# Optimization experiments

Measured on AMD Instinct MI355X. Metric: run time of the kernel, lower is better.

The kernel has to match this reference:

```python
import jax, jax.numpy as jnp
import numpy as np

B, T, D = 2, 2048, 1024
NH, DH = 16, 64  # inner = NH*DH = D
SCALE_INIT = 0.02


def setup_inputs() -> dict:
    key = jax.random.key(0)
    kx, kq, kk, kv, ko = jax.random.split(key, 5)
    return {
        "x": jax.random.normal(kx, (B, T, D), dtype=jnp.float32),
        "Wq": jax.random.normal(kq, (D, NH * DH), dtype=jnp.float32) * SCALE_INIT,
        "Wk": jax.random.normal(kk, (D, NH * DH), dtype=jnp.float32) * SCALE_INIT,
        "Wv": jax.random.normal(kv, (D, NH * DH), dtype=jnp.float32) * SCALE_INIT,
        "Wo": jax.random.normal(ko, (NH * DH, D), dtype=jnp.float32) * SCALE_INIT,
    }


def reference(x, Wq, Wk, Wv, Wo):
    # x: (B, T, D)
    b, t, _ = x.shape

    def split_heads(h):
        # (B, T, NH*DH) -> (B, NH, T, DH)
        return h.reshape(b, t, NH, DH).transpose(0, 2, 1, 3)

    q = split_heads(x @ Wq)
    k = split_heads(x @ Wk)
    v = split_heads(x @ Wv)

    scale = jnp.asarray(1.0 / np.sqrt(DH), dtype=x.dtype)
    # The per-chunk loop in the original is mathematically equivalent to
    # full causal attention: each query row attends to keys with k_pos <= q_pos.
    scores = jnp.einsum("bhqd,bhkd->bhqk", q, k) * scale  # (B, NH, T, T)
    causal_mask = jnp.arange(t)[None, :] > jnp.arange(t)[:, None]  # k_pos > q_pos
    scores = jnp.where(causal_mask, -jnp.inf, scores)
    attn = jax.nn.softmax(scores, axis=-1)
    attn = jnp.nan_to_num(attn)  # matches torch.nan_to_num (no fully-masked rows in causal case)
    o = jnp.einsum("bhqk,bhkd->bhqd", attn, v)  # (B, NH, T, DH)
    o = o.transpose(0, 2, 1, 3).reshape(b, t, NH * DH)  # merge heads
    return o @ Wo  # (B, T, D)
```

## Files before the change

### kernel.cpp

```cpp
#include <hip/hip_runtime.h>
#include <hip/hip_bf16.h>
#include <string.h>

#define Bsz 2
#define Tsz 2048
#define Dsz 1024
#define NHsz 16
#define Msz (Bsz*Tsz)

typedef unsigned short bfu;
typedef __attribute__((ext_vector_type(8))) short short8;
typedef __attribute__((ext_vector_type(4))) short short4v;
typedef __attribute__((ext_vector_type(4))) float floatx4;

__device__ __forceinline__ bfu f2bf(float f) {
  unsigned int u = __builtin_bit_cast(unsigned int, f);
  u += 0x7fffu + ((u >> 16) & 1u);
  return (bfu)(u >> 16);
}

__device__ __forceinline__ float fexp2(float x) {
#if __has_builtin(__builtin_amdgcn_exp2f)
  return __builtin_amdgcn_exp2f(x);
#else
  return exp2f(x);
#endif
}

__device__ __forceinline__ short4v pack4bf(float a, float b, float c_, float d) {
  __hip_bfloat162 h01 = __float22bfloat162_rn(make_float2(a, b));
  __hip_bfloat162 h23 = __float22bfloat162_rn(make_float2(c_, d));
  uint2 uu;
  memcpy(&uu.x, &h01, 4);
  memcpy(&uu.y, &h23, 4);
  return __builtin_bit_cast(short4v, uu);
}

__device__ __forceinline__ short8 pack8bf(float4 a, float4 b) {
  __hip_bfloat162 h0 = __float22bfloat162_rn(make_float2(a.x, a.y));
  __hip_bfloat162 h1 = __float22bfloat162_rn(make_float2(a.z, a.w));
  __hip_bfloat162 h2 = __float22bfloat162_rn(make_float2(b.x, b.y));
  __hip_bfloat162 h3 = __float22bfloat162_rn(make_float2(b.z, b.w));
  uint4 u;
  memcpy(&u.x, &h0, 4); memcpy(&u.y, &h1, 4);
  memcpy(&u.z, &h2, 4); memcpy(&u.w, &h3, 4);
  return __builtin_bit_cast(short8, u);
}

__device__ __forceinline__ void async16(const void* g, void* l) {
  void* gnc = (void*)g;
  __builtin_amdgcn_global_load_lds((__attribute__((address_space(1))) void*)gnc,
                                   (__attribute__((address_space(3))) void*)l,
                                   16, 0, 0);
}

__global__ __launch_bounds__(256) void transpose_w(const float* __restrict__ W0, const float* __restrict__ W1,
                                                   const float* __restrict__ W2, const float* __restrict__ W3,
                                                   bfu* __restrict__ wt,
                                                   const float* __restrict__ x, bfu* __restrict__ xb) {
  if (blockIdx.z == 4) {
    const int bf = (int)blockIdx.y * 32 + (int)blockIdx.x;
    const size_t i = ((size_t)bf * 256 + threadIdx.y * 32 + threadIdx.x) * 16;
    float4 a0 = *(const float4*)(x + i),     a1 = *(const float4*)(x + i + 4);
    float4 b0 = *(const float4*)(x + i + 8), b1 = *(const float4*)(x + i + 12);
    *(short8*)(xb + i)     = pack8bf(a0, a1);
    *(short8*)(xb + i + 8) = pack8bf(b0, b1);
    return;
  }
  __shared__ float tile[32][33];
  const float* W = blockIdx.z == 0 ? W0 : blockIdx.z == 1 ? W1 : blockIdx.z == 2 ? W2 : W3;
  const float s = (blockIdx.z == 0) ? 0.18033688011112042f : 1.0f;
  bfu* WT = wt + (size_t)blockIdx.z * Dsz * Dsz;
  int tx = threadIdx.x, ty = threadIdx.y;
  int kb = blockIdx.y * 32, nb = blockIdx.x * 32;
#pragma unroll
  for (int i = 0; i < 4; ++i)
    tile[ty + i*8][tx] = W[(size_t)(kb + ty + i*8) * Dsz + nb + tx];
  __syncthreads();
#pragma unroll
  for (int i = 0; i < 4; ++i)
    WT[(size_t)(nb + ty + i*8) * Dsz + kb + tx] = f2bf(tile[tx][ty + i*8] * s);
}

template <bool F32OUT, int NT>
__global__ __launch_bounds__(256) void gemm128(const bfu* __restrict__ Ain, const bfu* __restrict__ Bt0,
                                               void* __restrict__ C0, int K, int N,
                                               size_t strideB, size_t strideC) {
  constexpr int NJ = NT / 32;
  constexpr int LPS = 2 + NT / 64;
  const int tid = threadIdx.x, wave = tid >> 6, lane = tid & 63;
  const int g = lane >> 4, c = lane & 15;
  const int m0 = blockIdx.y * 128, n0 = blockIdx.x * NT;
  const bfu* Bt = Bt0 + strideB * blockIdx.z;
  __shared__ bfu smem[3][4096 + NT * 32];
  floatx4 acc[4][NJ] = {};
  const int srow = lane >> 2;
  const int scol = (((lane & 3) ^ ((lane >> 3) & 3)) << 3);
  const bfu* gB = Bt + (size_t)(n0 + srow) * K + scol;
  const bfu* gA = Ain + (size_t)(m0 + srow) * K + scol;
  const int wm = (wave >> 1) * 64, wn = (wave & 1) * (NT / 2);
  const int roct = (g ^ ((c >> 1) & 3)) << 3;

#define STAGE_G(buf, k0)                                                        \
  {                                                                             \
    _Pragma("unroll")                                                           \
    for (int cc = 0; cc < 2; ++cc) {                                            \
      const int chunk = wave * 2 + cc;                                          \
      async16(gA + (size_t)chunk * 16 * K + (k0), &smem[buf][chunk * 512]);     \
    }                                                                           \
    _Pragma("unroll")                                                           \
    for (int cc = 0; cc < NT / 64; ++cc) {                                      \
      const int chunk = wave * (NT / 64) + cc;                                  \
      async16(gB + (size_t)chunk * 16 * K + (k0), &smem[buf][4096 + chunk * 512]); \
    }                                                                           \
  }

  const int NK = K / 32;
  STAGE_G(0, 0);
  STAGE_G(1, 32);
  int buf = 0;
  for (int t = 0; t < NK; ++t) {
    if (t + 2 < NK) {
      const int nb = (buf + 2) >= 3 ? buf - 1 : buf + 2;
      STAGE_G(nb, (t + 2) * 32);
      asm volatile("s_waitcnt vmcnt(%0)" :: "i"(2 * LPS) : "memory");
    } else if (t + 1 < NK) {
      asm volatile("s_waitcnt vmcnt(%0)" :: "i"(LPS) : "memory");
    } else {
      asm volatile("s_waitcnt vmcnt(0)" ::: "memory");
    }
    __builtin_amdgcn_s_barrier();
    asm volatile("" ::: "memory");

    const bfu* AsC = &smem[buf][0];
    const bfu* BsC = &smem[buf][4096];
    short8 afr[4], bfr[NJ];
#pragma unroll
    for (int i = 0; i < 4; ++i) afr[i] = *(const short8*)&AsC[(wm + i*16 + c) * 32 + roct];
#pragma unroll
    for (int j = 0; j < NJ; ++j) bfr[j] = *(const short8*)&BsC[(wn + j*16 + c) * 32 + roct];
#pragma unroll
    for (int i = 0; i < 4; ++i)
#pragma unroll
      for (int j = 0; j < NJ; ++j)
        acc[i][j] = __builtin_amdgcn_mfma_f32_16x16x32_bf16(afr[i], bfr[j], acc[i][j], 0, 0, 0);

    asm volatile("" ::: "memory");
    __builtin_amdgcn_s_barrier();
    asm volatile("" ::: "memory");
    buf = (buf + 1 >= 3) ? 0 : buf + 1;
  }
#undef STAGE_G

  const bool vtrans = (!F32OUT) && (NT == 128) && (blockIdx.z == 2);
  if (vtrans) {
    bfu* sm = &smem[0][0];
    bfu* vtp = (bfu*)C0 + (size_t)2 * strideC;
#pragma unroll
    for (int p = 0; p < 2; ++p) {
      __syncthreads();
      if ((wave & 1) == p) {
#pragma unroll
        for (int i = 0; i < 4; ++i)
#pragma unroll
          for (int j = 0; j < NJ; ++j) {
            const int nl = j*16 + c;
            const int mg = ((wm + i*16) >> 3) + (g >> 1);
            const int phys = nl * 128 + ((mg ^ (nl & 15)) << 3) + ((g & 1) << 2);
            *(short4v*)&sm[phys] = pack4bf(acc[i][j][0], acc[i][j][1],
                                           acc[i][j][2], acc[i][j][3]);
          }
      }
      __syncthreads();
      const int h_ = (n0 + p * 64) >> 6;
      bfu* dst = vtp + ((size_t)((m0 >> 11) * 16 + h_) * 64) * Tsz + (m0 & 2047);
#pragma unroll
      for (int s = 0; s < 4; ++s) {
        const int nl = s * 16 + (tid >> 4);
        const int me = (tid & 15) << 3;
        const int phys = nl * 128 + (((me >> 3) ^ (nl & 15)) << 3);
        *(short8*)&dst[(size_t)nl * Tsz + me] = *(const short8*)&sm[phys];
      }
    }
    return;
  }

#pragma unroll
  for (int i = 0; i < 4; ++i) {
#pragma unroll
    for (int j = 0; j < NJ; ++j) {
      const int m = m0 + wm + i*16 + g*4;
      const int n = n0 + wn + j*16 + c;
#pragma unroll
      for (int r = 0; r < 4; ++r) {
        float v = acc[i][j][r];
        if (F32OUT) ((float*)C0)[(size_t)(m + r) * N + n] = v;
        else        ((bfu*)C0)[strideC * blockIdx.z + (size_t)(m + r) * N + n] = f2bf(v);
      }
    }
  }
}

__global__ __launch_bounds__(256, 4) void attn_kernel(const bfu* __restrict__ qkv,
                                                      float* __restrict__ op0,
                                                      float* __restrict__ op1,
                                                      float2* __restrict__ ml) {
  const int tid = threadIdx.x, wave = tid >> 6, lane = tid & 63;
  const int g = (lane >> 4) & 3, c = lane & 15, c7 = c & 7;

  const int flat = (int)blockIdx.y * 32 + (int)blockIdx.x;
  const int xcd = flat & 7, r_ = flat >> 3;
  const int ksplit = r_ & 1;
  const int s = (r_ >> 1) & 3, j0 = r_ >> 3;
  const int bh = xcd * 4 + s;
  const int b = bh >> 4, h = bh & 15;

  const size_t hbq = (size_t)b * Tsz * Dsz + h * 64;
  const bfu* Qp = qkv + hbq;
  const bfu* Kp = qkv + (size_t)Msz * Dsz + hbq;
  const bfu* Vt = qkv + (size_t)2 * Msz * Dsz + (size_t)bh * 64 * Tsz;
  float* op = ksplit ? op1 : op0;

  __shared__ bfu Ks[2][64 * 64];
  __shared__ bfu Vs[2][64 * 64];

  const int srow8 = lane >> 3;
  const int soff = ((lane & 7) ^ srow8) << 3;
  const floatx4 z4 = {0.0f, 0.0f, 0.0f, 0.0f};

  for (int hf = 0; hf < 2; ++hf) {
    const int j = hf ? (31 - j0) : j0;
    const int qw = j * 64 + wave * 16;

    short8 bq[2];
#pragma unroll
    for (int kk = 0; kk < 2; ++kk)
      bq[kk] = *(const short8*)(Qp + (size_t)(qw + c) * Dsz + kk * 32 + g * 8);

    floatx4 acc[4] = {};
    float mi = -3.0e38f, li = 0.0f;

    if (ksplit <= j) {
      const bfu* kpp[2]; const bfu* vpp[2];
#pragma unroll
      for (int cc = 0; cc < 2; ++cc) {
        const int ch = wave * 2 + cc;
        kpp[cc] = Kp + (size_t)(ksplit * 64 + ch * 8 + srow8) * Dsz + soff;
        vpp[cc] = Vt + (size_t)(ch * 8 + srow8) * Tsz + ksplit * 64 + soff;
      }

#pragma unroll
      for (int cc = 0; cc < 2; ++cc) {
        const int ch = wave * 2 + cc;
        async16(kpp[cc], &Ks[0][ch * 512]);
        async16(vpp[cc], &Vs[0][ch * 512]);
        kpp[cc] += (size_t)128 * Dsz;
        vpp[cc] += 128;
      }

      int cur = 0;
      for (int kt = ksplit; kt <= j; kt += 2) {
        if (kt + 2 <= j) {
#pragma unroll
          for (int cc = 0; cc < 2; ++cc) {
            const int ch = wave * 2 + cc;
            async16(kpp[cc], &Ks[cur ^ 1][ch * 512]);
            async16(vpp[cc], &Vs[cur ^ 1][ch * 512]);
            kpp[cc] += (size_t)128 * Dsz;
            vpp[cc] += 128;
          }
          asm volatile("s_waitcnt vmcnt(4)" ::: "memory");
        } else {
          asm volatile("s_waitcnt vmcnt(0)" ::: "memory");
        }
        __builtin_amdgcn_s_barrier();
        asm volatile("" ::: "memory");

        const bfu* KsC = &Ks[cur][0];
        const bfu* VsC = &Vs[cur][0];

        floatx4 st[4];
        __builtin_amdgcn_s_setprio(1);
#pragma unroll
        for (int mk = 0; mk < 4; ++mk) {
          const short8 kf = *(const short8*)&KsC[(mk * 16 + c) * 64 + ((g ^ c7) << 3)];
          st[mk] = __builtin_amdgcn_mfma_f32_16x16x32_bf16(kf, bq[0], z4, 0, 0, 0);
        }
#pragma unroll
        for (int mk = 0; mk < 4; ++mk) {
          const short8 kf = *(const short8*)&KsC[(mk * 16 + c) * 64 + (((4 + g) ^ c7) << 3)];
          st[mk] = __builtin_amdgcn_mfma_f32_16x16x32_bf16(kf, bq[1], st[mk], 0, 0, 0);
        }
        __builtin_amdgcn_s_setprio(0);

        if (kt == j) {
#pragma unroll
          for (int mk = 0; mk < 4; ++mk) {
            const int keyb = kt * 64 + mk * 16 + g * 4;
#pragma unroll
            for (int r = 0; r < 4; ++r)
              if (keyb + r > qw + c) st[mk][r] = -1.0e38f;
          }
        }

        float mloc = -3.0e38f;
#pragma unroll
        for (int mk = 0; mk < 4; ++mk)
          mloc = fmaxf(mloc, fmaxf(fmaxf(st[mk][0], st[mk][1]),
                                   fmaxf(st[mk][2], st[mk][3])));
        const bool resc = !__all(mloc <= mi + 8.0f);
        if (resc) {
          float mr = fmaxf(mloc, __shfl_xor(mloc, 16));
          mr = fmaxf(mr, __shfl_xor(mr, 32));
          const float mnew = fmaxf(mi, mr);
          const float alpha = fexp2(mi - mnew);
          li *= alpha;
          mi = mnew;
          float al[4];
#pragma unroll
          for (int rr = 0; rr < 4; ++rr) al[rr] = __shfl(alpha, (lane & 48) | (g * 4 + rr));
#pragma unroll
          for (int nd = 0; nd < 4; ++nd)
#pragma unroll
            for (int rr = 0; rr < 4; ++rr) acc[nd][rr] *= al[rr];
        }
        short4v pa[4];
#pragma unroll
        for (int mk = 0; mk < 4; ++mk) {
          const float p0 = fexp2(st[mk][0] - mi);
          const float p1 = fexp2(st[mk][1] - mi);
          const float p2 = fexp2(st[mk][2] - mi);
          const float p3 = fexp2(st[mk][3] - mi);
          li += (p0 + p1) + (p2 + p3);
          pa[mk] = pack4bf(p0, p1, p2, p3);
        }

        __builtin_amdgcn_s_setprio(1);
#pragma unroll
        for (int mk = 0; mk < 4; ++mk)
#pragma unroll
          for (int nd = 0; nd < 4; ++nd) {
            const short4v vf = *(const short4v*)&VsC[(nd * 16 + c) * 64 +
                ((((mk << 1) + (g >> 1)) ^ c7) << 3) + ((g & 1) << 2)];
            acc[nd] = __builtin_amdgcn_mfma_f32_16x16x16bf16_1k(pa[mk], vf, acc[nd], 0, 0, 0);
          }
        __builtin_amdgcn_s_setprio(0);

        asm volatile("" ::: "memory");
        __builtin_amdgcn_s_barrier();
        asm volatile("" ::: "memory");
        cur ^= 1;
      }
    }

    float lt = li;
    lt += __shfl_xor(lt, 16);
    lt += __shfl_xor(lt, 32);
#pragma unroll
    for (int rr = 0; rr < 4; ++rr) {
      const float lr = __shfl(lt, (lane & 48) | (g * 4 + rr));
      const float inv = lr > 0.0f ? 1.0f / lr : 0.0f;
#pragma unroll
      for (int nd = 0; nd < 4; ++nd)
        op[(size_t)(b * Tsz + qw + g * 4 + rr) * Dsz + h * 64 + nd * 16 + c] =
            acc[nd][rr] * inv;
    }
    if (lane < 16)
      ml[(size_t)ksplit * 65536 + bh * 2048 + qw + c] = make_float2(mi, lt);
  }
}

__global__ __launch_bounds__(256) void merge_split(const float* __restrict__ o0,
                                                   const float* __restrict__ o1,
                                                   const float2* __restrict__ ml,
                                                   bfu* __restrict__ ob) {
  const int idx = blockIdx.x * 256 + threadIdx.x;
  const int row = idx >> 7, ch = idx & 127;
  const int b = row >> 11, q = row & 2047;
  const int bh = b * 16 + (ch >> 3);
  const float2 a0 = ml[bh * 2048 + q];
  const float2 a1 = ml[65536 + bh * 2048 + q];
  const float M = fmaxf(a0.x, a1.x);
  const float w0 = fexp2(a0.x - M) * a0.y;
  const float w1 = fexp2(a1.x - M) * a1.y;
  const float inv = 1.0f / (w0 + w1);
  const float u0 = w0 * inv, u1 = w1 * inv;
  const size_t off = (size_t)row * 1024 + ch * 8;
  float4 p0 = *(const float4*)(o0 + off), q0 = *(const float4*)(o0 + off + 4);
  float4 p1 = *(const float4*)(o1 + off), q1 = *(const float4*)(o1 + off + 4);
  float4 ra, rb;
  ra.x = u0*p0.x + u1*p1.x; ra.y = u0*p0.y + u1*p1.y;
  ra.z = u0*p0.z + u1*p1.z; ra.w = u0*p0.w + u1*p1.w;
  rb.x = u0*q0.x + u1*q1.x; rb.y = u0*q0.y + u1*q1.y;
  rb.z = u0*q0.z + u1*q1.z; rb.w = u0*q0.w + u1*q1.w;
  *(short8*)(ob + off) = pack8bf(ra, rb);
}

extern "C" void kernel_launch(void* const* d_in, const int* in_sizes, int n_in,
                              void* d_out, int out_size, void* d_ws, size_t ws_size,
                              hipStream_t stream) {
  const float* x  = (const float*)d_in[0];
  const float* Wq = (const float*)d_in[1];
  const float* Wk = (const float*)d_in[2];
  const float* Wv = (const float*)d_in[3];
  const float* Wo = (const float*)d_in[4];
  float* out = (float*)d_out;

  bfu* wt    = (bfu*)d_ws;
  bfu* qkv   = wt + (size_t)4 * Dsz * Dsz;
  bfu* obuf  = qkv + (size_t)3 * Msz * Dsz;
  float* op0 = (float*)(obuf + (size_t)Msz * Dsz);
  float* op1 = op0 + (size_t)Msz * Dsz;
  float2* ml = (float2*)(op1 + (size_t)Msz * Dsz);

  transpose_w<<<dim3(32, 32, 5), dim3(32, 8), 0, stream>>>(Wq, Wk, Wv, Wo, wt, x, obuf);
  gemm128<false, 128><<<dim3(Dsz / 128, Msz / 128, 3), dim3(256), 0, stream>>>(
      obuf, wt, (void*)qkv, Dsz, Dsz, (size_t)Dsz * Dsz, (size_t)Msz * Dsz);
  attn_kernel<<<dim3(32, 32), dim3(256), 0, stream>>>(qkv, op0, op1, ml);
  merge_split<<<dim3(2048), dim3(256), 0, stream>>>(op0, op1, ml, obuf);
  gemm128<true, 64><<<dim3(Dsz / 64, Msz / 128, 1), dim3(256), 0, stream>>>(
      obuf, wt + (size_t)3 * Dsz * Dsz, (void*)out, Dsz, Dsz,
      (size_t)0, (size_t)0);
}
```

Before: 185.4 us.

## Load V fragments directly from global into registers, dropping LDS staging

The attention kernel no longer stages V tiles through shared memory. Each wave now reads its own V fragments from global memory into registers at the start of every key tile, and only K stays double-buffered in LDS. The K prefetch moves after the top-of-loop barrier, which allows the trailing per-iteration barrier to be removed. The aim is to save LDS traffic and a sync point. In exchange, every wave redundantly loads the whole V tile with narrow 8-byte strided global loads, and that latency must be hidden behind the QK MFMAs and the softmax.

```diff
diff --git a/kernel.cpp b/kernel.cpp
--- a/kernel.cpp
+++ b/kernel.cpp
@@ -222,7 +222,6 @@
   float* op = ksplit ? op1 : op0;
 
   __shared__ bfu Ks[2][64 * 64];
-  __shared__ bfu Vs[2][64 * 64];
 
   const int srow8 = lane >> 3;
   const int soff = ((lane & 7) ^ srow8) << 3;
@@ -241,43 +240,48 @@
     float mi = -3.0e38f, li = 0.0f;
 
     if (ksplit <= j) {
-      const bfu* kpp[2]; const bfu* vpp[2];
+      const bfu* kpp[2];
+      const bfu* vp[4];
+#pragma unroll
+      for (int cc = 0; cc < 2; ++cc)
+        kpp[cc] = Kp + (size_t)(ksplit * 64 + (wave * 2 + cc) * 8 + srow8) * Dsz + soff;
+#pragma unroll
+      for (int nd = 0; nd < 4; ++nd)
+        vp[nd] = Vt + (size_t)(nd * 16 + c) * Tsz + ksplit * 64 + 4 * g;
+
+      asm volatile("" ::: "memory");
+      __builtin_amdgcn_s_barrier();
+      asm volatile("" ::: "memory");
 #pragma unroll
       for (int cc = 0; cc < 2; ++cc) {
-        const int ch = wave * 2 + cc;
-        kpp[cc] = Kp + (size_t)(ksplit * 64 + ch * 8 + srow8) * Dsz + soff;
-        vpp[cc] = Vt + (size_t)(ch * 8 + srow8) * Tsz + ksplit * 64 + soff;
-      }
-
-#pragma unroll
-      for (int cc = 0; cc < 2; ++cc) {
-        const int ch = wave * 2 + cc;
-        async16(kpp[cc], &Ks[0][ch * 512]);
-        async16(vpp[cc], &Vs[0][ch * 512]);
+        async16(kpp[cc], &Ks[0][(wave * 2 + cc) * 512]);
         kpp[cc] += (size_t)128 * Dsz;
-        vpp[cc] += 128;
       }
 
       int cur = 0;
       for (int kt = ksplit; kt <= j; kt += 2) {
-        if (kt + 2 <= j) {
-#pragma unroll
-          for (int cc = 0; cc < 2; ++cc) {
-            const int ch = wave * 2 + cc;
-            async16(kpp[cc], &Ks[cur ^ 1][ch * 512]);
-            async16(vpp[cc], &Vs[cur ^ 1][ch * 512]);
-            kpp[cc] += (size_t)128 * Dsz;
-            vpp[cc] += 128;
-          }
-          asm volatile("s_waitcnt vmcnt(4)" ::: "memory");
-        } else {
-          asm volatile("s_waitcnt vmcnt(0)" ::: "memory");
-        }
+        asm volatile("s_waitcnt vmcnt(0)" ::: "memory");
         __builtin_amdgcn_s_barrier();
         asm volatile("" ::: "memory");
 
+        short4v vreg[4][4];
+#pragma unroll
+        for (int nd = 0; nd < 4; ++nd)
+#pragma unroll
+          for (int mk = 0; mk < 4; ++mk)
+            vreg[nd][mk] = *(const short4v*)(vp[nd] + 16 * mk);
+#pragma unroll
+        for (int nd = 0; nd < 4; ++nd) vp[nd] += 128;
+
+        if (kt + 2 <= j) {
+#pragma unroll
+          for (int cc = 0; cc < 2; ++cc) {
+            async16(kpp[cc], &Ks[cur ^ 1][(wave * 2 + cc) * 512]);
+            kpp[cc] += (size_t)128 * Dsz;
+          }
+        }
+
         const bfu* KsC = &Ks[cur][0];
-        const bfu* VsC = &Vs[cur][0];
 
         floatx4 st[4];
         __builtin_amdgcn_s_setprio(1);
@@ -339,16 +343,11 @@
 #pragma unroll
         for (int mk = 0; mk < 4; ++mk)
 #pragma unroll
-          for (int nd = 0; nd < 4; ++nd) {
-            const short4v vf = *(const short4v*)&VsC[(nd * 16 + c) * 64 +
-                ((((mk << 1) + (g >> 1)) ^ c7) << 3) + ((g & 1) << 2)];
-            acc[nd] = __builtin_amdgcn_mfma_f32_16x16x16bf16_1k(pa[mk], vf, acc[nd], 0, 0, 0);
-          }
+          for (int nd = 0; nd < 4; ++nd)
+            acc[nd] = __builtin_amdgcn_mfma_f32_16x16x16bf16_1k(pa[mk], vreg[nd][mk],
+                                                                acc[nd], 0, 0, 0);
         __builtin_amdgcn_s_setprio(0);
 
-        asm volatile("" ::: "memory");
-        __builtin_amdgcn_s_barrier();
-        asm volatile("" ::: "memory");
         cur ^= 1;
       }
     }
```

New measurement: 276.9 us. 1.49x slower.

## Fuse Q, K and V projections into one GEMM sharing each A tile

Applied to the files above, without the earlier changes.

Replaces the three-way batched QKV GEMM (128x128 tiles over z=3) with a dedicated kernel where each block computes a 128x64 tile of Q, K and V together. Each A tile is loaded once from global memory and reused against three weight tiles. The V transpose epilogue moves into the new kernel. Grid shape drops from 768 to 512 blocks, and the larger accumulator array and shared buffers raise register and LDS pressure, which may reduce occupancy.

```diff
diff --git a/kernel.cpp b/kernel.cpp
--- a/kernel.cpp
+++ b/kernel.cpp
@@ -80,6 +80,116 @@
 #pragma unroll
   for (int i = 0; i < 4; ++i)
     WT[(size_t)(nb + ty + i*8) * Dsz + kb + tx] = f2bf(tile[tx][ty + i*8] * s);
+}
+
+__global__ __launch_bounds__(256) void gemm_qkv(const bfu* __restrict__ Ain,
+                                                const bfu* __restrict__ wt,
+                                                bfu* __restrict__ out) {
+  const int tid = threadIdx.x, wave = tid >> 6, lane = tid & 63;
+  const int g = lane >> 4, c = lane & 15;
+  const int m0 = blockIdx.y * 128, n0 = blockIdx.x * 64;
+  __shared__ bfu smem[3][10240];
+  floatx4 acc[3][4][2] = {};
+  const int srow = lane >> 2;
+  const int scol = (((lane & 3) ^ ((lane >> 3) & 3)) << 3);
+  const bfu* gA = Ain + (size_t)(m0 + srow) * Dsz + scol;
+  const bfu* gB0 = wt + (size_t)(n0 + srow) * Dsz + scol;
+  const bfu* gB1 = gB0 + (size_t)Dsz * Dsz;
+  const bfu* gB2 = gB1 + (size_t)Dsz * Dsz;
+  const int wm = (wave >> 1) * 64, wn = (wave & 1) * 32;
+  const int roct = (g ^ ((c >> 1) & 3)) << 3;
+
+#define STAGE_Q(buf, k0)                                                        \
+  {                                                                             \
+    _Pragma("unroll")                                                           \
+    for (int cc = 0; cc < 2; ++cc) {                                            \
+      const int chunk = wave * 2 + cc;                                          \
+      async16(gA + (size_t)chunk * 16 * Dsz + (k0), &smem[buf][chunk * 512]);   \
+    }                                                                           \
+    async16(gB0 + (size_t)wave * 16 * Dsz + (k0), &smem[buf][4096 + wave * 512]); \
+    async16(gB1 + (size_t)wave * 16 * Dsz + (k0), &smem[buf][6144 + wave * 512]); \
+    async16(gB2 + (size_t)wave * 16 * Dsz + (k0), &smem[buf][8192 + wave * 512]); \
+  }
+
+  const int NK = Dsz / 32;
+  STAGE_Q(0, 0);
+  STAGE_Q(1, 32);
+  int buf = 0;
+  for (int t = 0; t < NK; ++t) {
+    if (t + 2 < NK) {
+      const int nb = (buf + 2) >= 3 ? buf - 1 : buf + 2;
+      STAGE_Q(nb, (t + 2) * 32);
+      asm volatile("s_waitcnt vmcnt(10)" ::: "memory");
+    } else if (t + 1 < NK) {
+      asm volatile("s_waitcnt vmcnt(5)" ::: "memory");
+    } else {
+      asm volatile("s_waitcnt vmcnt(0)" ::: "memory");
+    }
+    __builtin_amdgcn_s_barrier();
+    asm volatile("" ::: "memory");
+
+    const bfu* S = &smem[buf][0];
+    short8 afr[4], bfr[3][2];
+#pragma unroll
+    for (int i = 0; i < 4; ++i)
+      afr[i] = *(const short8*)&S[(wm + i*16 + c) * 32 + roct];
+#pragma unroll
+    for (int z = 0; z < 3; ++z)
+#pragma unroll
+      for (int j = 0; j < 2; ++j)
+        bfr[z][j] = *(const short8*)&S[4096 + z*2048 + (wn + j*16 + c) * 32 + roct];
+#pragma unroll
+    for (int z = 0; z < 3; ++z)
+#pragma unroll
+      for (int i = 0; i < 4; ++i)
+#pragma unroll
+        for (int j = 0; j < 2; ++j)
+          acc[z][i][j] = __builtin_amdgcn_mfma_f32_16x16x32_bf16(afr[i], bfr[z][j],
+                                                                 acc[z][i][j], 0, 0, 0);
+
+    asm volatile("" ::: "memory");
+    __builtin_amdgcn_s_barrier();
+    asm volatile("" ::: "memory");
+    buf = (buf + 1 >= 3) ? 0 : buf + 1;
+  }
+#undef STAGE_Q
+
+#pragma unroll
+  for (int z = 0; z < 2; ++z)
+#pragma unroll
+    for (int i = 0; i < 4; ++i)
+#pragma unroll
+      for (int j = 0; j < 2; ++j) {
+        const int m = m0 + wm + i*16 + g*4;
+        const int n = n0 + wn + j*16 + c;
+#pragma unroll
+        for (int r = 0; r < 4; ++r)
+          out[(size_t)z * Msz * Dsz + (size_t)(m + r) * Dsz + n] = f2bf(acc[z][i][j][r]);
+      }
+
+  __syncthreads();
+  bfu* sm = &smem[0][0];
+#pragma unroll
+  for (int i = 0; i < 4; ++i)
+#pragma unroll
+    for (int j = 0; j < 2; ++j) {
+      const int d = wn + j*16 + c;
+      const int mg = ((wm + i*16) >> 3) + (g >> 1);
+      const int phys = d * 128 + ((mg ^ (d & 15)) << 3) + ((g & 1) << 2);
+      *(short4v*)&sm[phys] = pack4bf(acc[2][i][j][0], acc[2][i][j][1],
+                                     acc[2][i][j][2], acc[2][i][j][3]);
+    }
+  __syncthreads();
+  const int h_ = n0 >> 6;
+  bfu* dst = out + (size_t)2 * Msz * Dsz +
+             ((size_t)((m0 >> 11) * 16 + h_) * 64) * Tsz + (m0 & 2047);
+#pragma unroll
+  for (int s = 0; s < 4; ++s) {
+    const int nl = s * 16 + (tid >> 4);
+    const int me = (tid & 15) << 3;
+    const int phys = nl * 128 + (((me >> 3) ^ (nl & 15)) << 3);
+    *(short8*)&dst[(size_t)nl * Tsz + me] = *(const short8*)&sm[phys];
+  }
 }
 
 template <bool F32OUT, int NT>
@@ -151,39 +261,6 @@
     buf = (buf + 1 >= 3) ? 0 : buf + 1;
   }
 #undef STAGE_G
-
-  const bool vtrans = (!F32OUT) && (NT == 128) && (blockIdx.z == 2);
-  if (vtrans) {
-    bfu* sm = &smem[0][0];
-    bfu* vtp = (bfu*)C0 + (size_t)2 * strideC;
-#pragma unroll
-    for (int p = 0; p < 2; ++p) {
-      __syncthreads();
-      if ((wave & 1) == p) {
-#pragma unroll
-        for (int i = 0; i < 4; ++i)
-#pragma unroll
-          for (int j = 0; j < NJ; ++j) {
-            const int nl = j*16 + c;
-            const int mg = ((wm + i*16) >> 3) + (g >> 1);
-            const int phys = nl * 128 + ((mg ^ (nl & 15)) << 3) + ((g & 1) << 2);
-            *(short4v*)&sm[phys] = pack4bf(acc[i][j][0], acc[i][j][1],
-                                           acc[i][j][2], acc[i][j][3]);
-          }
-      }
-      __syncthreads();
-      const int h_ = (n0 + p * 64) >> 6;
-      bfu* dst = vtp + ((size_t)((m0 >> 11) * 16 + h_) * 64) * Tsz + (m0 & 2047);
-#pragma unroll
-      for (int s = 0; s < 4; ++s) {
-        const int nl = s * 16 + (tid >> 4);
-        const int me = (tid & 15) << 3;
-        const int phys = nl * 128 + (((me >> 3) ^ (nl & 15)) << 3);
-        *(short8*)&dst[(size_t)nl * Tsz + me] = *(const short8*)&sm[phys];
-      }
-    }
-    return;
-  }
 
 #pragma unroll
   for (int i = 0; i < 4; ++i) {
@@ -414,8 +491,7 @@
   float2* ml = (float2*)(op1 + (size_t)Msz * Dsz);
 
   transpose_w<<<dim3(32, 32, 5), dim3(32, 8), 0, stream>>>(Wq, Wk, Wv, Wo, wt, x, obuf);
-  gemm128<false, 128><<<dim3(Dsz / 128, Msz / 128, 3), dim3(256), 0, stream>>>(
-      obuf, wt, (void*)qkv, Dsz, Dsz, (size_t)Dsz * Dsz, (size_t)Msz * Dsz);
+  gemm_qkv<<<dim3(16, 32), dim3(256), 0, stream>>>(obuf, wt, qkv);
   attn_kernel<<<dim3(32, 32), dim3(256), 0, stream>>>(qkv, op0, op1, ml);
   merge_split<<<dim3(2048), dim3(256), 0, stream>>>(op0, op1, ml, obuf);
   gemm128<true, 64><<<dim3(Dsz / 64, Msz / 128, 1), dim3(256), 0, stream>>>(
```

Result: no change. 184.4 us (-0.5%).
